# Performance work log

Hardware: AMD Instinct MI355X
Metric: run time of the kernel (lower is better)

## Reference

```python
import jax, jax.numpy as jnp
import numpy as np

B, S, D, H = 2, 2048, 1024, 16
HS = D // H
SCALE = 1.0 / float(np.sqrt(HS))


def setup_inputs() -> dict:
    key = jax.random.key(0)
    ks = jax.random.split(key, 11)
    w_std = 1.0 / float(np.sqrt(D))  # ~ nn.Linear init scale
    inp = {
        "queries": jax.random.normal(ks[0], (B, S, D), dtype=jnp.float32),
        "keys": jax.random.normal(ks[1], (B, S, D), dtype=jnp.float32),
        "values": jax.random.normal(ks[2], (B, S, D), dtype=jnp.float32),
        "Wq": jax.random.normal(ks[3], (D, D), dtype=jnp.float32) * w_std,
        "bq": jax.random.normal(ks[4], (D,), dtype=jnp.float32) * w_std,
        "Wk": jax.random.normal(ks[5], (D, D), dtype=jnp.float32) * w_std,
        "bk": jax.random.normal(ks[6], (D,), dtype=jnp.float32) * w_std,
        "Wv": jax.random.normal(ks[7], (D, D), dtype=jnp.float32) * w_std,
        "bv": jax.random.normal(ks[8], (D,), dtype=jnp.float32) * w_std,
        "Wo": jax.random.normal(ks[9], (D, D), dtype=jnp.float32) * w_std,
        "bo": jax.random.normal(ks[10], (D,), dtype=jnp.float32) * w_std,
    }
    return inp


def _split_heads(x):
    # (B,S,D) -> (B,H,S,HS)
    return x.reshape(B, S, H, HS).transpose(0, 2, 1, 3)


def reference(queries, keys, values, Wq, bq, Wk, bk, Wv, bv, Wo, bo):
    # nn.Linear: y = x @ W^T + b
    q = _split_heads(queries @ Wq.T + bq)
    k = _split_heads(keys @ Wk.T + bk)
    v = _split_heads(values @ Wv.T + bv)

    scores = jnp.einsum("bhqd,bhkd->bhqk", q, k) * SCALE  # (B,H,S,S)
    causal = jnp.tril(jnp.ones((S, S), dtype=bool))
    scores = jnp.where(causal, scores, jnp.float32(-1e9))  # masked_fill(-1e9)
    attn = jax.nn.softmax(scores, axis=-1)

    attended = jnp.einsum("bhqk,bhkd->bhqd", attn, v)  # (B,H,S,HS)
    # Faithful to original: .view(B, -1, H*HS) on the contiguous (B,H,S,HS)
    # tensor WITHOUT transposing heads back -> plain row-major reshape.
    outputs = attended.reshape(B, S, H * HS)
    return outputs @ Wo.T + bo
```

## Files before the change

kernel.cpp:

```cpp
#include <hip/hip_runtime.h>
#include <hip/hip_bf16.h>

typedef unsigned short u16;
typedef unsigned int   u32;
typedef __attribute__((ext_vector_type(8))) short bf16x8;
typedef __attribute__((ext_vector_type(4))) float f32x4;
typedef __attribute__((ext_vector_type(4))) float f4v;
typedef __attribute__((ext_vector_type(4))) u16  u16x4;

#define BB 2
#define SS 2048
#define DD 1024
#define HH 16
#define NT 4096
#define ATT_SCALE 0.125f

__device__ __forceinline__ u16 f2bf(float f) {
  union { float f; u32 u; } c; c.f = f;
  u32 u = c.u + 0x7fffu + ((c.u >> 16) & 1u);
  return (u16)(u >> 16);
}

__device__ __forceinline__ void gload_lds16(const void* g, void* l) {
  __builtin_amdgcn_global_load_lds(
      (const __attribute__((address_space(1))) u32*)g,
      (__attribute__((address_space(3))) u32*)l, 16, 0, 0);
}

__global__ void cvt_bf16_kernel(const float* __restrict__ s0, const float* __restrict__ s1,
                                const float* __restrict__ s2, const float* __restrict__ s3,
                                u16* __restrict__ d0, u16* __restrict__ d1,
                                u16* __restrict__ d2, u16* __restrict__ d3, int n4) {
  const int z = blockIdx.y;
  const float* s = (z == 0) ? s0 : (z == 1) ? s1 : (z == 2) ? s2 : s3;
  u16* d = (z == 0) ? d0 : (z == 1) ? d1 : (z == 2) ? d2 : d3;
  int i = blockIdx.x * blockDim.x + threadIdx.x;
  int stride = gridDim.x * blockDim.x;
  for (int k = i; k < n4; k += stride) {
    f4v v = ((const f4v*)s)[k];
    u16x4 o;
    o[0] = f2bf(v[0]); o[1] = f2bf(v[1]); o[2] = f2bf(v[2]); o[3] = f2bf(v[3]);
    ((u16x4*)d)[k] = o;
  }
}

template<int OUT_F32, int BIAS_ROW>
__global__ __launch_bounds__(256, 2) void gemm_bt_kernel(
    const u16* __restrict__ A0, const u16* __restrict__ A1, const u16* __restrict__ A2,
    const u16* __restrict__ W0, const u16* __restrict__ W1, const u16* __restrict__ W2,
    const float* __restrict__ b0, const float* __restrict__ b1, const float* __restrict__ b2,
    void* __restrict__ C0, void* __restrict__ C1, void* __restrict__ C2,
    int M, int N, int K) {
  const int z = blockIdx.z;
  const u16* A = (z == 0) ? A0 : (z == 1) ? A1 : A2;
  const u16* W = (z == 0) ? W0 : (z == 1) ? W1 : W2;
  const float* bias = (z == 0) ? b0 : (z == 1) ? b1 : b2;
  void* Cp = (z == 0) ? C0 : (z == 1) ? C1 : C2;

  __shared__ u16 As[128 * 64];
  __shared__ u16 Bs[128 * 64];
  const int t = threadIdx.x;
  const int lane = t & 63, w = t >> 6;
  const int wr = w >> 1, wc = w & 1;
  const int l15 = lane & 15, l4 = lane >> 4;
  const int m0 = blockIdx.x * 128, n0 = blockIdx.y * 128;

  f32x4 acc[4][4];
#pragma unroll
  for (int m = 0; m < 4; ++m)
#pragma unroll
    for (int n = 0; n < 4; ++n) acc[m][n] = (f32x4)(0.0f);

  const u16* aSrc[4];
  const u16* bSrc[4];
#pragma unroll
  for (int i = 0; i < 4; ++i) {
    int c = i * 256 + t, row = c >> 3, gg = (c & 7) ^ (row & 7);
    aSrc[i] = A + (size_t)(m0 + row) * K + gg * 8;
    bSrc[i] = W + (size_t)(n0 + row) * K + gg * 8;
  }

  const int nk = K >> 6;
  for (int kt = 0; kt < nk; ++kt) {
    __syncthreads();
#pragma unroll
    for (int i = 0; i < 4; ++i) {
      gload_lds16(aSrc[i] + kt * 64, &As[i * 2048 + w * 512]);
      gload_lds16(bSrc[i] + kt * 64, &Bs[i * 2048 + w * 512]);
    }
    __syncthreads();
    bf16x8 af[4][2], bfr[4][2];
#pragma unroll
    for (int m = 0; m < 4; ++m) {
      int row = wr * 64 + m * 16 + l15;
#pragma unroll
      for (int kf = 0; kf < 2; ++kf)
        af[m][kf] = *(const bf16x8*)&As[row * 64 + ((kf * 4 + l4) ^ (row & 7)) * 8];
    }
#pragma unroll
    for (int n = 0; n < 4; ++n) {
      int row = wc * 64 + n * 16 + l15;
#pragma unroll
      for (int kf = 0; kf < 2; ++kf)
        bfr[n][kf] = *(const bf16x8*)&Bs[row * 64 + ((kf * 4 + l4) ^ (row & 7)) * 8];
    }
#pragma unroll
    for (int kf = 0; kf < 2; ++kf)
#pragma unroll
      for (int m = 0; m < 4; ++m)
#pragma unroll
        for (int n = 0; n < 4; ++n)
          acc[m][n] = __builtin_amdgcn_mfma_f32_16x16x32_bf16(af[m][kf], bfr[n][kf], acc[m][n], 0, 0, 0);
  }

  float bvc[4];
#pragma unroll
  for (int n = 0; n < 4; ++n)
    bvc[n] = BIAS_ROW ? 0.0f : bias[n0 + wc * 64 + n * 16 + l15];
#pragma unroll
  for (int m = 0; m < 4; ++m) {
#pragma unroll
    for (int j = 0; j < 4; ++j) {
      int r = m0 + wr * 64 + m * 16 + l4 * 4 + j;
      float br = BIAS_ROW ? bias[r] : 0.0f;
#pragma unroll
      for (int n = 0; n < 4; ++n) {
        int cc = n0 + wc * 64 + n * 16 + l15;
        float v = acc[m][n][j] + (BIAS_ROW ? br : bvc[n]);
        if (OUT_F32) ((float*)Cp)[(size_t)r * N + cc] = v;
        else         ((u16*)Cp)[(size_t)r * N + cc] = f2bf(v);
      }
    }
  }
}

__global__ __launch_bounds__(64, 2) void attn_kernel(
    const u16* __restrict__ Qb, const u16* __restrict__ Kb,
    const u16* __restrict__ VtT, u16* __restrict__ Xb) {
  __shared__ u16 Pl[16 * 72];

  const int p = blockIdx.x;
  const int bh = blockIdx.y;
  const int b = bh >> 4, h = bh & 15;
  const int lane = threadIdx.x & 63;
  const int l15 = lane & 15, l4 = lane >> 4;

  const u16* Kbase = Kb + (size_t)b * SS * DD + h * 64;
  const u16* Vbase = VtT + (size_t)h * 64 * NT + (size_t)b * SS;

  bf16x8 onesf;
#pragma unroll
  for (int e = 0; e < 8; ++e) onesf[e] = (l15 == 0) ? (short)0x3F80 : (short)0;

  for (int si = 0; si < 2; ++si) {
    const int qt = si ? (127 - p) : p;
    const int q0 = qt * 16;

    bf16x8 aq[2];
#pragma unroll
    for (int kf = 0; kf < 2; ++kf)
      aq[kf] = *(const bf16x8*)&Qb[((size_t)b * SS + q0 + l15) * DD + h * 64 + kf * 32 + l4 * 8];

    f32x4 acc[4], accsum;
    float mrun[4];
#pragma unroll
    for (int x = 0; x < 4; ++x) { acc[x] = (f32x4)(0.0f); mrun[x] = -3.0e38f; }
    accsum = (f32x4)(0.0f);

    auto loadK = [&](int kt, bf16x8 kfr[4][2]) {
      const int k0 = kt * 64;
#pragma unroll
      for (int nf = 0; nf < 4; ++nf) {
        const u16* kr = Kbase + (size_t)(k0 + nf * 16 + l15) * DD + l4 * 8;
        kfr[nf][0] = *(const bf16x8*)kr;
        kfr[nf][1] = *(const bf16x8*)(kr + 32);
      }
    };

    auto compute = [&](int kt, bf16x8 kfr[4][2]) {
      const int k0 = kt * 64;
      f32x4 s[4];
#pragma unroll
      for (int nf = 0; nf < 4; ++nf) s[nf] = (f32x4)(0.0f);

      __builtin_amdgcn_s_setprio(1);
#pragma unroll
      for (int nf = 0; nf < 4; ++nf)
#pragma unroll
        for (int kf = 0; kf < 2; ++kf)
          s[nf] = __builtin_amdgcn_mfma_f32_16x16x32_bf16(aq[kf], kfr[nf][kf], s[nf], 0, 0, 0);
      __builtin_amdgcn_s_setprio(0);

      bf16x8 vf[4][2];
#pragma unroll
      for (int nd = 0; nd < 4; ++nd) {
        const u16* vr = Vbase + (size_t)(nd * 16 + l15) * NT + k0 + l4 * 8;
        vf[nd][0] = *(const bf16x8*)vr;
        vf[nd][1] = *(const bf16x8*)(vr + 32);
      }

      const bool need_mask = (k0 + 63 > q0);
#pragma unroll
      for (int nf = 0; nf < 4; ++nf)
#pragma unroll
        for (int j = 0; j < 4; ++j) {
          float v = s[nf][j] * ATT_SCALE;
          if (need_mask) {
            int key = k0 + nf * 16 + l15;
            int qrow = q0 + l4 * 4 + j;
            if (key > qrow) v = -1.0e9f;
          }
          s[nf][j] = v;
        }

      float pmax[4];
#pragma unroll
      for (int j = 0; j < 4; ++j) {
        float v = fmaxf(fmaxf(s[0][j], s[1][j]), fmaxf(s[2][j], s[3][j]));
        v = fmaxf(v, __shfl_xor(v, 1));
        v = fmaxf(v, __shfl_xor(v, 2));
        v = fmaxf(v, __shfl_xor(v, 4));
        v = fmaxf(v, __shfl_xor(v, 8));
        pmax[j] = v;
      }

      int ok = 1;
#pragma unroll
      for (int j = 0; j < 4; ++j) ok &= (pmax[j] - mrun[j] <= 8.0f) ? 1 : 0;
      if (!__all(ok)) {
#pragma unroll
        for (int j = 0; j < 4; ++j) {
          float mnew = fmaxf(mrun[j], pmax[j]);
          float sc = __expf(mrun[j] - mnew);
          mrun[j] = mnew;
          accsum[j] *= sc;
#pragma unroll
          for (int nd = 0; nd < 4; ++nd) acc[nd][j] *= sc;
        }
      }

#pragma unroll
      for (int nf = 0; nf < 4; ++nf)
#pragma unroll
        for (int j = 0; j < 4; ++j)
          s[nf][j] = __expf(s[nf][j] - mrun[j]);

#pragma unroll
      for (int nf = 0; nf < 4; ++nf)
#pragma unroll
        for (int j = 0; j < 4; ++j)
          Pl[(l4 * 4 + j) * 72 + nf * 16 + l15] = f2bf(s[nf][j]);

      bf16x8 ap[2];
#pragma unroll
      for (int kf = 0; kf < 2; ++kf)
        ap[kf] = *(const bf16x8*)&Pl[l15 * 72 + kf * 32 + l4 * 8];

      __builtin_amdgcn_s_setprio(1);
#pragma unroll
      for (int nd = 0; nd < 4; ++nd)
#pragma unroll
        for (int kf = 0; kf < 2; ++kf)
          acc[nd] = __builtin_amdgcn_mfma_f32_16x16x32_bf16(ap[kf], vf[nd][kf], acc[nd], 0, 0, 0);
#pragma unroll
      for (int kf = 0; kf < 2; ++kf)
        accsum = __builtin_amdgcn_mfma_f32_16x16x32_bf16(ap[kf], onesf, accsum, 0, 0, 0);
      __builtin_amdgcn_s_setprio(0);
    };

    const int nkt = (qt >> 2) + 1;
    bf16x8 kA[4][2], kB[4][2];
    loadK(0, kA);
    for (int kt = 0; kt < nkt;) {
      if (kt + 1 < nkt) loadK(kt + 1, kB);
      compute(kt, kA);
      ++kt;
      if (kt >= nkt) break;
      if (kt + 1 < nkt) loadK(kt + 1, kA);
      compute(kt, kB);
      ++kt;
    }

#pragma unroll
    for (int j = 0; j < 4; ++j) {
      float lsum = __shfl(accsum[j], l4 * 16);
      float inv = 1.0f / lsum;
      int srow = q0 + l4 * 4 + j;
      size_t base = (size_t)b * SS * DD + (size_t)h * SS * 64 + (size_t)srow * 64;
#pragma unroll
      for (int nd = 0; nd < 4; ++nd)
        Xb[base + nd * 16 + l15] = f2bf(acc[nd][j] * inv);
    }
  }
}

extern "C" void kernel_launch(void* const* d_in, const int* in_sizes, int n_in,
                              void* d_out, int out_size, void* d_ws, size_t ws_size,
                              hipStream_t stream) {
  const float* q_in = (const float*)d_in[0];
  const float* k_in = (const float*)d_in[1];
  const float* v_in = (const float*)d_in[2];
  const float* Wq = (const float*)d_in[3];
  const float* bq = (const float*)d_in[4];
  const float* Wk = (const float*)d_in[5];
  const float* bk = (const float*)d_in[6];
  const float* Wv = (const float*)d_in[7];
  const float* bv = (const float*)d_in[8];
  const float* Wo = (const float*)d_in[9];
  const float* bo = (const float*)d_in[10];

  char* ws = (char*)d_ws;
  const size_t SZ_IN = (size_t)BB * SS * DD * 2;
  const size_t SZ_W = (size_t)DD * DD * 2;
  u16* qb  = (u16*)(ws);
  u16* kb  = (u16*)(ws + SZ_IN);
  u16* vb  = (u16*)(ws + 2 * SZ_IN);
  u16* wqb = (u16*)(ws + 3 * SZ_IN);
  u16* wkb = (u16*)(ws + 3 * SZ_IN + SZ_W);
  u16* wvb = (u16*)(ws + 3 * SZ_IN + 2 * SZ_W);
  u16* wob = (u16*)(ws + 3 * SZ_IN + 3 * SZ_W);
  u16* Qb  = (u16*)(ws + 3 * SZ_IN + 4 * SZ_W);
  u16* Kb  = (u16*)(ws + 4 * SZ_IN + 4 * SZ_W);
  u16* VtT = (u16*)(ws + 5 * SZ_IN + 4 * SZ_W);
  u16* Xb  = (u16*)(ws + 6 * SZ_IN + 4 * SZ_W);

  cvt_bf16_kernel<<<dim3(2048, 3), 256, 0, stream>>>(q_in, k_in, v_in, nullptr,
                                                     qb, kb, vb, nullptr, (BB * SS * DD) / 4);
  cvt_bf16_kernel<<<dim3(1024, 4), 256, 0, stream>>>(Wq, Wk, Wv, Wo,
                                                     wqb, wkb, wvb, wob, (DD * DD) / 4);

  gemm_bt_kernel<0, 0><<<dim3(32, 8, 2), 256, 0, stream>>>(
      qb, kb, nullptr, wqb, wkb, nullptr, bq, bk, nullptr, Qb, Kb, nullptr, NT, DD, DD);

  gemm_bt_kernel<0, 1><<<dim3(8, 32, 1), 256, 0, stream>>>(
      wvb, nullptr, nullptr, vb, nullptr, nullptr, bv, nullptr, nullptr,
      VtT, nullptr, nullptr, DD, NT, DD);

  attn_kernel<<<dim3(64, BB * HH), 64, 0, stream>>>(Qb, Kb, VtT, Xb);

  gemm_bt_kernel<1, 0><<<dim3(32, 8, 1), 256, 0, stream>>>(
      Xb, nullptr, nullptr, wob, nullptr, nullptr, bo, nullptr, nullptr,
      d_out, nullptr, nullptr, NT, DD, DD);
}
```

Before: 314.7 us.

## Merge QKV projections into one launch and widen attention tiles to 32 queries

```diff
diff --git a/kernel.cpp b/kernel.cpp
--- a/kernel.cpp
+++ b/kernel.cpp
@@ -44,18 +44,22 @@
   }
 }
 
-template<int OUT_F32, int BIAS_ROW>
+template<int OUT_F32>
 __global__ __launch_bounds__(256, 2) void gemm_bt_kernel(
     const u16* __restrict__ A0, const u16* __restrict__ A1, const u16* __restrict__ A2,
     const u16* __restrict__ W0, const u16* __restrict__ W1, const u16* __restrict__ W2,
     const float* __restrict__ b0, const float* __restrict__ b1, const float* __restrict__ b2,
     void* __restrict__ C0, void* __restrict__ C1, void* __restrict__ C2,
-    int M, int N, int K) {
+    int K) {
   const int z = blockIdx.z;
   const u16* A = (z == 0) ? A0 : (z == 1) ? A1 : A2;
   const u16* W = (z == 0) ? W0 : (z == 1) ? W1 : W2;
   const float* bias = (z == 0) ? b0 : (z == 1) ? b1 : b2;
   void* Cp = (z == 0) ? C0 : (z == 1) ? C1 : C2;
+  const int bias_row = (z == 2);
+  const int Nn = (z == 2) ? NT : DD;
+  const int m0 = ((z == 2) ? blockIdx.y : blockIdx.x) * 128;
+  const int n0 = ((z == 2) ? blockIdx.x : blockIdx.y) * 128;
 
   __shared__ u16 As[128 * 64];
   __shared__ u16 Bs[128 * 64];
@@ -63,7 +67,6 @@
   const int lane = t & 63, w = t >> 6;
   const int wr = w >> 1, wc = w & 1;
   const int l15 = lane & 15, l4 = lane >> 4;
-  const int m0 = blockIdx.x * 128, n0 = blockIdx.y * 128;
 
   f32x4 acc[4][4];
 #pragma unroll
@@ -116,19 +119,19 @@
   float bvc[4];
 #pragma unroll
   for (int n = 0; n < 4; ++n)
-    bvc[n] = BIAS_ROW ? 0.0f : bias[n0 + wc * 64 + n * 16 + l15];
+    bvc[n] = bias_row ? 0.0f : bias[n0 + wc * 64 + n * 16 + l15];
 #pragma unroll
   for (int m = 0; m < 4; ++m) {
 #pragma unroll
     for (int j = 0; j < 4; ++j) {
       int r = m0 + wr * 64 + m * 16 + l4 * 4 + j;
-      float br = BIAS_ROW ? bias[r] : 0.0f;
+      float br = bias_row ? bias[r] : 0.0f;
 #pragma unroll
       for (int n = 0; n < 4; ++n) {
         int cc = n0 + wc * 64 + n * 16 + l15;
-        float v = acc[m][n][j] + (BIAS_ROW ? br : bvc[n]);
-        if (OUT_F32) ((float*)Cp)[(size_t)r * N + cc] = v;
-        else         ((u16*)Cp)[(size_t)r * N + cc] = f2bf(v);
+        float v = acc[m][n][j] + (bias_row ? br : bvc[n]);
+        if (OUT_F32) ((float*)Cp)[(size_t)r * Nn + cc] = v;
+        else         ((u16*)Cp)[(size_t)r * Nn + cc] = f2bf(v);
       }
     }
   }
@@ -137,14 +140,24 @@
 __global__ __launch_bounds__(64, 2) void attn_kernel(
     const u16* __restrict__ Qb, const u16* __restrict__ Kb,
     const u16* __restrict__ VtT, u16* __restrict__ Xb) {
-  __shared__ u16 Pl[16 * 72];
-
-  const int p = blockIdx.x;
-  const int bh = blockIdx.y;
+  __shared__ u16 Pl[32 * 72];
+
+  const int x = blockIdx.x;
+  const int bh = x & 31;
+  const int qt = 63 - (x >> 5);
   const int b = bh >> 4, h = bh & 15;
+  const int q0 = qt * 32;
   const int lane = threadIdx.x & 63;
   const int l15 = lane & 15, l4 = lane >> 4;
 
+  bf16x8 aq[2][2];
+#pragma unroll
+  for (int mf = 0; mf < 2; ++mf)
+#pragma unroll
+    for (int kf = 0; kf < 2; ++kf)
+      aq[mf][kf] = *(const bf16x8*)&Qb[((size_t)b * SS + q0 + mf * 16 + l15) * DD +
+                                       h * 64 + kf * 32 + l4 * 8];
+
   const u16* Kbase = Kb + (size_t)b * SS * DD + h * 64;
   const u16* Vbase = VtT + (size_t)h * 64 * NT + (size_t)b * SS;
 
@@ -152,146 +165,164 @@
 #pragma unroll
   for (int e = 0; e < 8; ++e) onesf[e] = (l15 == 0) ? (short)0x3F80 : (short)0;
 
-  for (int si = 0; si < 2; ++si) {
-    const int qt = si ? (127 - p) : p;
-    const int q0 = qt * 16;
-
-    bf16x8 aq[2];
-#pragma unroll
-    for (int kf = 0; kf < 2; ++kf)
-      aq[kf] = *(const bf16x8*)&Qb[((size_t)b * SS + q0 + l15) * DD + h * 64 + kf * 32 + l4 * 8];
-
-    f32x4 acc[4], accsum;
-    float mrun[4];
-#pragma unroll
-    for (int x = 0; x < 4; ++x) { acc[x] = (f32x4)(0.0f); mrun[x] = -3.0e38f; }
-    accsum = (f32x4)(0.0f);
-
-    auto loadK = [&](int kt, bf16x8 kfr[4][2]) {
-      const int k0 = kt * 64;
-#pragma unroll
-      for (int nf = 0; nf < 4; ++nf) {
-        const u16* kr = Kbase + (size_t)(k0 + nf * 16 + l15) * DD + l4 * 8;
-        kfr[nf][0] = *(const bf16x8*)kr;
-        kfr[nf][1] = *(const bf16x8*)(kr + 32);
-      }
-    };
-
-    auto compute = [&](int kt, bf16x8 kfr[4][2]) {
-      const int k0 = kt * 64;
-      f32x4 s[4];
-#pragma unroll
-      for (int nf = 0; nf < 4; ++nf) s[nf] = (f32x4)(0.0f);
-
-      __builtin_amdgcn_s_setprio(1);
+  f32x4 acc[2][4], accsum[2];
+  float mrun[2][4];
+#pragma unroll
+  for (int mf = 0; mf < 2; ++mf) {
+    accsum[mf] = (f32x4)(0.0f);
+#pragma unroll
+    for (int xk = 0; xk < 4; ++xk) { acc[mf][xk] = (f32x4)(0.0f); mrun[mf][xk] = -3.0e38f; }
+  }
+
+  auto loadK = [&](int kt, bf16x8 kfr[4][2]) {
+    const int k0 = kt * 64;
+#pragma unroll
+    for (int nf = 0; nf < 4; ++nf) {
+      const u16* kr = Kbase + (size_t)(k0 + nf * 16 + l15) * DD + l4 * 8;
+      kfr[nf][0] = *(const bf16x8*)kr;
+      kfr[nf][1] = *(const bf16x8*)(kr + 32);
+    }
+  };
+
+  auto compute = [&](int kt, bf16x8 kfr[4][2]) {
+    const int k0 = kt * 64;
+    f32x4 s[2][4];
+#pragma unroll
+    for (int mf = 0; mf < 2; ++mf)
+#pragma unroll
+      for (int nf = 0; nf < 4; ++nf) s[mf][nf] = (f32x4)(0.0f);
+
+    __builtin_amdgcn_s_setprio(1);
+#pragma unroll
+    for (int nf = 0; nf < 4; ++nf)
+#pragma unroll
+      for (int kf = 0; kf < 2; ++kf)
+#pragma unroll
+        for (int mf = 0; mf < 2; ++mf)
+          s[mf][nf] = __builtin_amdgcn_mfma_f32_16x16x32_bf16(aq[mf][kf], kfr[nf][kf], s[mf][nf], 0, 0, 0);
+    __builtin_amdgcn_s_setprio(0);
+
+    bf16x8 vf[4][2];
+#pragma unroll
+    for (int nd = 0; nd < 4; ++nd) {
+      const u16* vr = Vbase + (size_t)(nd * 16 + l15) * NT + k0 + l4 * 8;
+      vf[nd][0] = *(const bf16x8*)vr;
+      vf[nd][1] = *(const bf16x8*)(vr + 32);
+    }
+
+#pragma unroll
+    for (int mf = 0; mf < 2; ++mf) {
+      const bool need_mask = (k0 + 63 > q0 + mf * 16);
 #pragma unroll
       for (int nf = 0; nf < 4; ++nf)
 #pragma unroll
-        for (int kf = 0; kf < 2; ++kf)
-          s[nf] = __builtin_amdgcn_mfma_f32_16x16x32_bf16(aq[kf], kfr[nf][kf], s[nf], 0, 0, 0);
-      __builtin_amdgcn_s_setprio(0);
-
-      bf16x8 vf[4][2];
-#pragma unroll
-      for (int nd = 0; nd < 4; ++nd) {
-        const u16* vr = Vbase + (size_t)(nd * 16 + l15) * NT + k0 + l4 * 8;
-        vf[nd][0] = *(const bf16x8*)vr;
-        vf[nd][1] = *(const bf16x8*)(vr + 32);
-      }
-
-      const bool need_mask = (k0 + 63 > q0);
-#pragma unroll
-      for (int nf = 0; nf < 4; ++nf)
-#pragma unroll
         for (int j = 0; j < 4; ++j) {
-          float v = s[nf][j] * ATT_SCALE;
+          float v = s[mf][nf][j] * ATT_SCALE;
           if (need_mask) {
             int key = k0 + nf * 16 + l15;
-            int qrow = q0 + l4 * 4 + j;
+            int qrow = q0 + mf * 16 + l4 * 4 + j;
             if (key > qrow) v = -1.0e9f;
           }
-          s[nf][j] = v;
+          s[mf][nf][j] = v;
         }
-
-      float pmax[4];
+    }
+
+    float pmax[2][4];
+#pragma unroll
+    for (int mf = 0; mf < 2; ++mf)
 #pragma unroll
       for (int j = 0; j < 4; ++j) {
-        float v = fmaxf(fmaxf(s[0][j], s[1][j]), fmaxf(s[2][j], s[3][j]));
+        float v = fmaxf(fmaxf(s[mf][0][j], s[mf][1][j]), fmaxf(s[mf][2][j], s[mf][3][j]));
         v = fmaxf(v, __shfl_xor(v, 1));
         v = fmaxf(v, __shfl_xor(v, 2));
         v = fmaxf(v, __shfl_xor(v, 4));
         v = fmaxf(v, __shfl_xor(v, 8));
-        pmax[j] = v;
+        pmax[mf][j] = v;
       }
 
-      int ok = 1;
-#pragma unroll
-      for (int j = 0; j < 4; ++j) ok &= (pmax[j] - mrun[j] <= 8.0f) ? 1 : 0;
-      if (!__all(ok)) {
+    int ok = 1;
+#pragma unroll
+    for (int mf = 0; mf < 2; ++mf)
+#pragma unroll
+      for (int j = 0; j < 4; ++j) ok &= (pmax[mf][j] - mrun[mf][j] <= 8.0f) ? 1 : 0;
+    if (!__all(ok)) {
+#pragma unroll
+      for (int mf = 0; mf < 2; ++mf)
 #pragma unroll
         for (int j = 0; j < 4; ++j) {
-          float mnew = fmaxf(mrun[j], pmax[j]);
-          float sc = __expf(mrun[j] - mnew);
-          mrun[j] = mnew;
-          accsum[j] *= sc;
-#pragma unroll
-          for (int nd = 0; nd < 4; ++nd) acc[nd][j] *= sc;
+          float mnew = fmaxf(mrun[mf][j], pmax[mf][j]);
+          float sc = __expf(mrun[mf][j] - mnew);
+          mrun[mf][j] = mnew;
+          accsum[mf][j] *= sc;
+#pragma unroll
+          for (int nd = 0; nd < 4; ++nd) acc[mf][nd][j] *= sc;
         }
-      }
-
+    }
+
+#pragma unroll
+    for (int mf = 0; mf < 2; ++mf)
 #pragma unroll
       for (int nf = 0; nf < 4; ++nf)
 #pragma unroll
         for (int j = 0; j < 4; ++j)
-          s[nf][j] = __expf(s[nf][j] - mrun[j]);
-
+          s[mf][nf][j] = __expf(s[mf][nf][j] - mrun[mf][j]);
+
+#pragma unroll
+    for (int mf = 0; mf < 2; ++mf)
 #pragma unroll
       for (int nf = 0; nf < 4; ++nf)
 #pragma unroll
         for (int j = 0; j < 4; ++j)
-          Pl[(l4 * 4 + j) * 72 + nf * 16 + l15] = f2bf(s[nf][j]);
-
-      bf16x8 ap[2];
-#pragma unroll
-      for (int kf = 0; kf < 2; ++kf)
-        ap[kf] = *(const bf16x8*)&Pl[l15 * 72 + kf * 32 + l4 * 8];
-
-      __builtin_amdgcn_s_setprio(1);
+          Pl[(mf * 16 + l4 * 4 + j) * 72 + nf * 16 + l15] = f2bf(s[mf][nf][j]);
+
+    bf16x8 ap[2][2];
+#pragma unroll
+    for (int mf = 0; mf < 2; ++mf)
+#pragma unroll
+      for (int kf = 0; kf < 2; ++kf)
+        ap[mf][kf] = *(const bf16x8*)&Pl[(mf * 16 + l15) * 72 + kf * 32 + l4 * 8];
+
+    __builtin_amdgcn_s_setprio(1);
+#pragma unroll
+    for (int nd = 0; nd < 4; ++nd)
+#pragma unroll
+      for (int kf = 0; kf < 2; ++kf)
+#pragma unroll
+        for (int mf = 0; mf < 2; ++mf)
+          acc[mf][nd] = __builtin_amdgcn_mfma_f32_16x16x32_bf16(ap[mf][kf], vf[nd][kf], acc[mf][nd], 0, 0, 0);
+#pragma unroll
+    for (int mf = 0; mf < 2; ++mf)
+#pragma unroll
+      for (int kf = 0; kf < 2; ++kf)
+        accsum[mf] = __builtin_amdgcn_mfma_f32_16x16x32_bf16(ap[mf][kf], onesf, accsum[mf], 0, 0, 0);
+    __builtin_amdgcn_s_setprio(0);
+  };
+
+  const int nkt = (qt >> 1) + 1;
+  bf16x8 kA[4][2], kB[4][2];
+  loadK(0, kA);
+  for (int kt = 0; kt < nkt;) {
+    if (kt + 1 < nkt) loadK(kt + 1, kB);
+    compute(kt, kA);
+    ++kt;
+    if (kt >= nkt) break;
+    if (kt + 1 < nkt) loadK(kt + 1, kA);
+    compute(kt, kB);
+    ++kt;
+  }
+
+#pragma unroll
+  for (int mf = 0; mf < 2; ++mf)
+#pragma unroll
+    for (int j = 0; j < 4; ++j) {
+      float lsum = __shfl(accsum[mf][j], l4 * 16);
+      float inv = 1.0f / lsum;
+      int srow = q0 + mf * 16 + l4 * 4 + j;
+      size_t base = (size_t)b * SS * DD + (size_t)h * SS * 64 + (size_t)srow * 64;
 #pragma unroll
       for (int nd = 0; nd < 4; ++nd)
-#pragma unroll
-        for (int kf = 0; kf < 2; ++kf)
-          acc[nd] = __builtin_amdgcn_mfma_f32_16x16x32_bf16(ap[kf], vf[nd][kf], acc[nd], 0, 0, 0);
-#pragma unroll
-      for (int kf = 0; kf < 2; ++kf)
-        accsum = __builtin_amdgcn_mfma_f32_16x16x32_bf16(ap[kf], onesf, accsum, 0, 0, 0);
-      __builtin_amdgcn_s_setprio(0);
-    };
-
-    const int nkt = (qt >> 2) + 1;
-    bf16x8 kA[4][2], kB[4][2];
-    loadK(0, kA);
-    for (int kt = 0; kt < nkt;) {
-      if (kt + 1 < nkt) loadK(kt + 1, kB);
-      compute(kt, kA);
-      ++kt;
-      if (kt >= nkt) break;
-      if (kt + 1 < nkt) loadK(kt + 1, kA);
-      compute(kt, kB);
-      ++kt;
-    }
-
-#pragma unroll
-    for (int j = 0; j < 4; ++j) {
-      float lsum = __shfl(accsum[j], l4 * 16);
-      float inv = 1.0f / lsum;
-      int srow = q0 + l4 * 4 + j;
-      size_t base = (size_t)b * SS * DD + (size_t)h * SS * 64 + (size_t)srow * 64;
-#pragma unroll
-      for (int nd = 0; nd < 4; ++nd)
-        Xb[base + nd * 16 + l15] = f2bf(acc[nd][j] * inv);
-    }
-  }
+        Xb[base + nd * 16 + l15] = f2bf(acc[mf][nd][j] * inv);
+    }
 }
 
 extern "C" void kernel_launch(void* const* d_in, const int* in_sizes, int n_in,
@@ -329,16 +360,12 @@
   cvt_bf16_kernel<<<dim3(1024, 4), 256, 0, stream>>>(Wq, Wk, Wv, Wo,
                                                      wqb, wkb, wvb, wob, (DD * DD) / 4);
 
-  gemm_bt_kernel<0, 0><<<dim3(32, 8, 2), 256, 0, stream>>>(
-      qb, kb, nullptr, wqb, wkb, nullptr, bq, bk, nullptr, Qb, Kb, nullptr, NT, DD, DD);
-
-  gemm_bt_kernel<0, 1><<<dim3(8, 32, 1), 256, 0, stream>>>(
-      wvb, nullptr, nullptr, vb, nullptr, nullptr, bv, nullptr, nullptr,
-      VtT, nullptr, nullptr, DD, NT, DD);
-
-  attn_kernel<<<dim3(64, BB * HH), 64, 0, stream>>>(Qb, Kb, VtT, Xb);
-
-  gemm_bt_kernel<1, 0><<<dim3(32, 8, 1), 256, 0, stream>>>(
+  gemm_bt_kernel<0><<<dim3(32, 8, 3), 256, 0, stream>>>(
+      qb, kb, wvb, wqb, wkb, vb, bq, bk, bv, Qb, Kb, VtT, DD);
+
+  attn_kernel<<<dim3(64 * 32), 64, 0, stream>>>(Qb, Kb, VtT, Xb);
+
+  gemm_bt_kernel<1><<<dim3(32, 8, 1), 256, 0, stream>>>(
       Xb, nullptr, nullptr, wob, nullptr, nullptr, bo, nullptr, nullptr,
-      d_out, nullptr, nullptr, NT, DD, DD);
-}
+      d_out, nullptr, nullptr, DD);
+}
```

Result: faster. 303.2 us (-3.7%).
